# Kernel optimization log

Hardware: AMD Instinct MI355X
Metric: run time of the kernel (lower is better)

## Reference

```python
import jax, jax.numpy as jnp
import numpy as np

MD = 4  # max displacement -> (2*MD+1)**2 = 81 output channels

def setup_inputs() -> dict:
    key = jax.random.key(0)
    k1, k2 = jax.random.split(key)
    B, C, H, W = 4, 128, 128, 256
    t1 = jax.random.normal(k1, (B, C, H, W), dtype=jnp.float32)
    t2 = jax.random.normal(k2, (B, C, H, W), dtype=jnp.float32)
    return {"t1": t1, "t2": t2}

def reference(t1, t2):
    # PWC-Net correlation: for each displacement (dy,dx) in [-MD,MD]^2,
    # corr[b, d, y, x] = mean_c t1[b,c,y,x] * t2[b,c,y+dy,x+dx]
    B, C, H, W = t1.shape
    t2p = jnp.pad(t2, ((0, 0), (0, 0), (MD, MD), (MD, MD)))
    outs = []
    for dy in range(2 * MD + 1):
        for dx in range(2 * MD + 1):
            shifted = t2p[:, :, dy:dy + H, dx:dx + W]  # (B,C,H,W)
            outs.append(jnp.mean(t1 * shifted, axis=1))  # (B,H,W)
    return jnp.stack(outs, axis=1)  # (B, 81, H, W)
```

## Files before the change

kernel.cpp:

```cpp
#include <hip/hip_runtime.h>

#define MD   4
#define B_   4
#define C_   128
#define H_   128
#define W_   256
#define ND   9

typedef float  float4v __attribute__((ext_vector_type(4)));
typedef float  f32x4   __attribute__((ext_vector_type(4)));
typedef short  bf16x8  __attribute__((ext_vector_type(8)));
typedef unsigned int u32;
typedef u32    u32x4   __attribute__((ext_vector_type(4)));

#define TS ((size_t)B_ * H_ * 4 * W_ * 32)

static __device__ __forceinline__ unsigned short f2bf(float f) {
    u32 u = __float_as_uint(f);
    u32 r = (u + 0x7fffu + ((u >> 16) & 1u)) >> 16;
    return (unsigned short)r;
}

__global__ __launch_bounds__(256, 2)
void convert_one(const float* __restrict__ src0,
                 unsigned short* __restrict__ dst0) {
    const int bid = blockIdx.x;
    const int kc  = bid & 3;
    const int y   = (bid >> 2) & (H_ - 1);
    const int b   = bid >> 9;
    const int x   = threadIdx.x;
    const float* src = src0 + ((size_t)(b * C_ + kc * 32) * H_ + y) * W_ + x;
    const size_t hw = (size_t)H_ * W_;

    float f[32];
    #pragma unroll
    for (int k = 0; k < 32; ++k) f[k] = src[(size_t)k * hw];

    unsigned short* dst =
        dst0 + ((((size_t)(b * H_ + y)) * 4 + kc) * W_ + x) * 32;
    #pragma unroll
    for (int q = 0; q < 4; ++q) {
        u32x4 pk;
        #pragma unroll
        for (int j = 0; j < 4; ++j)
            pk[j] = (u32)f2bf(f[q * 8 + 2 * j]) |
                    ((u32)f2bf(f[q * 8 + 2 * j + 1]) << 16);
        *(u32x4*)(dst + q * 8) = pk;
    }
}

__global__ __launch_bounds__(512, 2)
void corr_mfma7(const float* __restrict__ t1,
                const unsigned short* __restrict__ t2w,
                float* __restrict__ out) {
    __shared__ float scr[8][2 * 16 * 33];
    __shared__ __align__(16) unsigned short aS[2][2][128][32];

    const int tid = threadIdx.x;
    const int l   = tid & 63;
    const int w   = tid >> 6;
    const int bid = blockIdx.x;
    const int xcd = bid & 7;
    const int xh  = xcd >> 2;
    const int ypq = xcd & 3;
    const int rst = bid >> 3;
    const int b   = rst >> 4;
    const int yp  = ypq * 16 + (rst & 15);
    const int y0  = yp * 2;
    const int ln  = l & 15;
    const int kg  = l >> 4;
    const int X0  = (xh * 8 + w) * 16;
    const float scale = 1.0f / (float)C_;
    const bf16x8 z8 = (bf16x8)(short)0;
    const size_t hw = (size_t)H_ * W_;

    const int q  = tid >> 7;
    const int xl = tid & 127;

    f32x4 aA0[ND], aA1[ND], aB0[ND], aB1[ND];
    #pragma unroll
    for (int r = 0; r < ND; ++r) {
        aA0[r] = (f32x4)0.0f; aA1[r] = (f32x4)0.0f;
        aB0[r] = (f32x4)0.0f; aB1[r] = (f32x4)0.0f;
    }

    int col0 = X0 - 8 + ln;
    int col1 = X0 + 8 + ln;
    const bool ob0 = col0 < 0;
    const bool ob1 = col1 > W_ - 1;
    col0 = ob0 ? 0 : col0;
    col1 = ob1 ? W_ - 1 : col1;

    float f[16];
#define ALOAD(kc_)                                                          \
    {                                                                       \
        _Pragma("unroll")                                                   \
        for (int i = 0; i < 16; ++i) {                                      \
            const int cl = (i >> 1) + 8 * q;                                \
            const int yy_ = i & 1;                                          \
            f[i] = t1[((size_t)(b * C_ + (kc_) * 32 + cl) * H_              \
                       + y0 + yy_) * W_ + xh * 128 + xl];                   \
        }                                                                   \
    }
#define AWRITE(buf_)                                                        \
    {                                                                       \
        bf16x8 w0, w1;                                                      \
        _Pragma("unroll")                                                   \
        for (int j = 0; j < 8; ++j) {                                       \
            w0[j] = (short)f2bf(f[2 * j]);                                  \
            w1[j] = (short)f2bf(f[2 * j + 1]);                              \
        }                                                                   \
        *(bf16x8*)&aS[buf_][0][xl][q * 8] = w0;                             \
        *(bf16x8*)&aS[buf_][1][xl][q * 8] = w1;                             \
    }

    ALOAD(0);
    AWRITE(0);
    __syncthreads();

    #pragma unroll
    for (int kc = 0; kc < 4; ++kc) {
        const int buf = kc & 1;
        if (kc < 3) ALOAD(kc + 1);

        const bf16x8 fA = *(const bf16x8*)&aS[buf][0][w * 16 + ln][kg * 8];
        const bf16x8 fB = *(const bf16x8*)&aS[buf][1][w * 16 + ln][kg * 8];

        #pragma unroll
        for (int r = 0; r < ND + 1; ++r) {
            const int row = y0 + r - MD;
            if (0 <= row && row < H_) {
                const unsigned short* b_base =
                    t2w + ((((size_t)(b * H_ + row)) * 4 + kc) * W_) * 32;
                bf16x8 b0 = *(const bf16x8*)(b_base + (size_t)col0 * 32 + kg * 8);
                bf16x8 b1 = *(const bf16x8*)(b_base + (size_t)col1 * 32 + kg * 8);
                b0 = ob0 ? z8 : b0;
                b1 = ob1 ? z8 : b1;
                if (r < ND) {
                    aA0[r] = __builtin_amdgcn_mfma_f32_16x16x32_bf16(fA, b0, aA0[r], 0, 0, 0);
                    aA1[r] = __builtin_amdgcn_mfma_f32_16x16x32_bf16(fA, b1, aA1[r], 0, 0, 0);
                }
                if (r >= 1) {
                    aB0[r-1] = __builtin_amdgcn_mfma_f32_16x16x32_bf16(fB, b0, aB0[r-1], 0, 0, 0);
                    aB1[r-1] = __builtin_amdgcn_mfma_f32_16x16x32_bf16(fB, b1, aB1[r-1], 0, 0, 0);
                }
            }
        }

        if (kc < 3) AWRITE(buf ^ 1);
        __syncthreads();
    }
#undef ALOAD
#undef AWRITE

    float* sw = scr[w];

    #pragma unroll
    for (int r = 0; r < ND; ++r) {
        const int row = y0 + r - MD;
        const bool liv = (0 <= row && row < H_);
        #pragma unroll
        for (int i = 0; i < 4; ++i) {
            sw[(kg * 4 + i) * 33 + ln]       = aA0[r][i];
            sw[528 + (kg * 4 + i) * 33 + ln] = aA1[r][i];
        }
        #pragma unroll
        for (int i = 0; i < 3; ++i) {
            const int dx = i * 4 + kg;
            if (dx < ND) {
                const int m  = ln;
                const int md = m + dx;
                const int idx = (md < 12) ? (m * 33 + md + 4)
                                          : (528 + m * 33 + md - 12);
                const float v = liv ? sw[idx] * scale : 0.0f;
                out[((((size_t)b * 81) + r * ND + dx) * H_ + y0) * W_ + X0 + m] = v;
            }
        }
    }
    #pragma unroll
    for (int r = 0; r < ND; ++r) {
        const int row = y0 + 1 + r - MD;
        const bool liv = (0 <= row && row < H_);
        #pragma unroll
        for (int i = 0; i < 4; ++i) {
            sw[(kg * 4 + i) * 33 + ln]       = aB0[r][i];
            sw[528 + (kg * 4 + i) * 33 + ln] = aB1[r][i];
        }
        #pragma unroll
        for (int i = 0; i < 3; ++i) {
            const int dx = i * 4 + kg;
            if (dx < ND) {
                const int m  = ln;
                const int md = m + dx;
                const int idx = (md < 12) ? (m * 33 + md + 4)
                                          : (528 + m * 33 + md - 12);
                const float v = liv ? sw[idx] * scale : 0.0f;
                out[((((size_t)b * 81) + r * ND + dx) * H_ + (y0 + 1)) * W_ + X0 + m] = v;
            }
        }
    }
}

__global__ __launch_bounds__(9 * 64, 3)
void corr_fallback(const float* __restrict__ t1,
                   const float* __restrict__ t2,
                   float* __restrict__ out) {
    const int tid  = threadIdx.x;
    const int lane = tid & 63;
    const int w    = tid >> 6;
    const int bid  = blockIdx.x;
    const int swz  = (bid & 7) * 32 + (bid >> 3);
    const int yp   = swz & 63;
    const int b    = swz >> 6;
    const int y0   = yp * 2;
    const int half = lane >> 5;
    const int lx   = lane & 31;
    const int x0   = lx * 8;
    const int yrow = y0 + half;
    const int yy   = yrow + w - MD;
    const bool live = (0 <= yy) && (yy < H_);
    const int  yc  = yy < 0 ? 0 : (yy > H_ - 1 ? H_ - 1 : yy);
    const float sc = live ? (1.0f / (float)C_) : 0.0f;
    const bool lm  = (lx == 0);
    const bool rm  = (lx == 31);
    const int offL = lm ? 0 : -4;
    const int offR = rm ? 0 :  8;

    float acc[ND][8];
    #pragma unroll
    for (int dx = 0; dx < ND; ++dx)
        #pragma unroll
        for (int j = 0; j < 8; ++j) acc[dx][j] = 0.0f;

    const float* p1 = t1 + (((size_t)(b * C_)) * H_ + yrow) * W_ + x0;
    const float* p2 = t2 + (((size_t)(b * C_)) * H_ + yc  ) * W_ + x0;
    const size_t chstr = (size_t)H_ * W_;

    #pragma unroll 2
    for (int c = 0; c < C_; ++c) {
        const float* pc1 = p1 + (size_t)c * chstr;
        const float* pc2 = p2 + (size_t)c * chstr;
        const float4v a0 = *(const float4v*)(pc1);
        const float4v a1 = *(const float4v*)(pc1 + 4);
        float4v wl = *(const float4v*)(pc2 + offL);
        const float4v v0 = *(const float4v*)(pc2);
        const float4v v1 = *(const float4v*)(pc2 + 4);
        float4v wr = *(const float4v*)(pc2 + offR);
        #pragma unroll
        for (int qq = 0; qq < 4; ++qq) {
            wl[qq] = lm ? 0.0f : wl[qq];
            wr[qq] = rm ? 0.0f : wr[qq];
        }
        float win[16];
        #pragma unroll
        for (int qq = 0; qq < 4; ++qq) {
            win[qq] = wl[qq]; win[4 + qq] = v0[qq];
            win[8 + qq] = v1[qq]; win[12 + qq] = wr[qq];
        }
        #pragma unroll
        for (int dx = 0; dx < ND; ++dx)
            #pragma unroll
            for (int j = 0; j < 8; ++j) {
                const float aj = (j < 4) ? a0[j] : a1[j - 4];
                acc[dx][j] = fmaf(aj, win[dx + j], acc[dx][j]);
            }
    }

    #pragma unroll
    for (int dx = 0; dx < ND; ++dx) {
        float4v o0, o1;
        #pragma unroll
        for (int j = 0; j < 4; ++j) {
            o0[j] = acc[dx][j] * sc;
            o1[j] = acc[dx][4 + j] * sc;
        }
        const size_t oidx =
            (((size_t)(b * ND * ND) + w * ND + dx) * H_ + yrow) * W_ + x0;
        *(float4v*)&out[oidx]     = o0;
        *(float4v*)&out[oidx + 4] = o1;
    }
}

extern "C" void kernel_launch(void* const* d_in, const int* in_sizes, int n_in,
                              void* d_out, int out_size, void* d_ws, size_t ws_size,
                              hipStream_t stream) {
    const float* t1 = (const float*)d_in[0];
    const float* t2 = (const float*)d_in[1];
    float* out      = (float*)d_out;
    const size_t need = TS * sizeof(unsigned short);
    if (ws_size >= need) {
        unsigned short* ws = (unsigned short*)d_ws;
        convert_one<<<dim3(B_ * H_ * 4), 256, 0, stream>>>(t2, ws);
        corr_mfma7 <<<dim3(B_ * H_), 512, 0, stream>>>(t1, ws, out);
    } else {
        corr_fallback<<<dim3(B_ * H_ / 2), 9 * 64, 0, stream>>>(t1, t2, out);
    }
}
```

Measured before the change: 69.03 us.

## Vectorize t1 staging loads, single-buffer padded LDS, and vectorize output stores

The t1 tile is now read with float4 loads over 8 consecutive x positions, where it used to be read with scalar per-channel loads. It is packed as bf16 channel pairs into a single padded LDS buffer, replacing the double buffer, and an extra barrier guards reuse of that buffer. The epilogue stages each displacement row in LDS so it can be written out with float4 stores instead of scalar stores. The aim is to cut global load and store instruction counts and LDS use, at the cost of one more __syncthreads per chunk and less overlap between staging and MFMA work.

```diff
diff --git a/kernel.cpp b/kernel.cpp
--- a/kernel.cpp
+++ b/kernel.cpp
@@ -50,11 +50,11 @@
 }
 
 __global__ __launch_bounds__(512, 2)
-void corr_mfma7(const float* __restrict__ t1,
+void corr_mfma8(const float* __restrict__ t1,
                 const unsigned short* __restrict__ t2w,
                 float* __restrict__ out) {
-    __shared__ float scr[8][2 * 16 * 33];
-    __shared__ __align__(16) unsigned short aS[2][2][128][32];
+    __shared__ u32   aS[2][128][20];
+    __shared__ float scr[8][16 * 36 + 9 * 16];
 
     const int tid = threadIdx.x;
     const int l   = tid & 63;
@@ -74,8 +74,31 @@
     const bf16x8 z8 = (bf16x8)(short)0;
     const size_t hw = (size_t)H_ * W_;
 
-    const int q  = tid >> 7;
-    const int xl = tid & 127;
+    const int cpair = tid & 15;
+    const int ys    = (tid >> 4) & 1;
+    const int xoct  = tid >> 5;
+    const int gx    = xh * 128 + xoct * 8;
+
+    float fst[16];
+#define ALOAD(kc_)                                                         \
+    {                                                                      \
+        const float* s0 = t1 + ((size_t)(b * C_ + (kc_) * 32 + 2 * cpair)  \
+                                * H_ + y0 + ys) * W_ + gx;                 \
+        const float* s1 = s0 + hw;                                         \
+        *(float4v*)&fst[0]  = *(const float4v*)(s0);                       \
+        *(float4v*)&fst[4]  = *(const float4v*)(s0 + 4);                   \
+        *(float4v*)&fst[8]  = *(const float4v*)(s1);                       \
+        *(float4v*)&fst[12] = *(const float4v*)(s1 + 4);                   \
+    }
+#define AWRITE()                                                           \
+    {                                                                      \
+        _Pragma("unroll")                                                  \
+        for (int j = 0; j < 8; ++j) {                                      \
+            const u32 pk = (u32)f2bf(fst[j]) |                             \
+                           ((u32)f2bf(fst[8 + j]) << 16);                  \
+            aS[ys][xoct * 8 + j][cpair] = pk;                              \
+        }                                                                  \
+    }
 
     f32x4 aA0[ND], aA1[ND], aB0[ND], aB1[ND];
     #pragma unroll
@@ -91,40 +114,14 @@
     col0 = ob0 ? 0 : col0;
     col1 = ob1 ? W_ - 1 : col1;
 
-    float f[16];
-#define ALOAD(kc_)                                                          \
-    {                                                                       \
-        _Pragma("unroll")                                                   \
-        for (int i = 0; i < 16; ++i) {                                      \
-            const int cl = (i >> 1) + 8 * q;                                \
-            const int yy_ = i & 1;                                          \
-            f[i] = t1[((size_t)(b * C_ + (kc_) * 32 + cl) * H_              \
-                       + y0 + yy_) * W_ + xh * 128 + xl];                   \
-        }                                                                   \
-    }
-#define AWRITE(buf_)                                                        \
-    {                                                                       \
-        bf16x8 w0, w1;                                                      \
-        _Pragma("unroll")                                                   \
-        for (int j = 0; j < 8; ++j) {                                       \
-            w0[j] = (short)f2bf(f[2 * j]);                                  \
-            w1[j] = (short)f2bf(f[2 * j + 1]);                              \
-        }                                                                   \
-        *(bf16x8*)&aS[buf_][0][xl][q * 8] = w0;                             \
-        *(bf16x8*)&aS[buf_][1][xl][q * 8] = w1;                             \
-    }
-
-    ALOAD(0);
-    AWRITE(0);
+    ALOAD(0); AWRITE();
     __syncthreads();
 
     #pragma unroll
     for (int kc = 0; kc < 4; ++kc) {
-        const int buf = kc & 1;
+        const bf16x8 fA = *(const bf16x8*)&aS[0][w * 16 + ln][kg * 4];
+        const bf16x8 fB = *(const bf16x8*)&aS[1][w * 16 + ln][kg * 4];
         if (kc < 3) ALOAD(kc + 1);
-
-        const bf16x8 fA = *(const bf16x8*)&aS[buf][0][w * 16 + ln][kg * 8];
-        const bf16x8 fB = *(const bf16x8*)&aS[buf][1][w * 16 + ln][kg * 8];
 
         #pragma unroll
         for (int r = 0; r < ND + 1; ++r) {
@@ -147,13 +144,15 @@
             }
         }
 
-        if (kc < 3) AWRITE(buf ^ 1);
+        __syncthreads();
+        if (kc < 3) { AWRITE(); }
         __syncthreads();
     }
 #undef ALOAD
 #undef AWRITE
 
     float* sw = scr[w];
+    float* sb = sw + 16 * 36;
 
     #pragma unroll
     for (int r = 0; r < ND; ++r) {
@@ -161,20 +160,22 @@
         const bool liv = (0 <= row && row < H_);
         #pragma unroll
         for (int i = 0; i < 4; ++i) {
-            sw[(kg * 4 + i) * 33 + ln]       = aA0[r][i];
-            sw[528 + (kg * 4 + i) * 33 + ln] = aA1[r][i];
+            sw[(kg * 4 + i) * 36 + ln]      = aA0[r][i];
+            sw[(kg * 4 + i) * 36 + 16 + ln] = aA1[r][i];
         }
         #pragma unroll
         for (int i = 0; i < 3; ++i) {
             const int dx = i * 4 + kg;
             if (dx < ND) {
-                const int m  = ln;
-                const int md = m + dx;
-                const int idx = (md < 12) ? (m * 33 + md + 4)
-                                          : (528 + m * 33 + md - 12);
-                const float v = liv ? sw[idx] * scale : 0.0f;
-                out[((((size_t)b * 81) + r * ND + dx) * H_ + y0) * W_ + X0 + m] = v;
+                const float v = liv ? sw[ln * 36 + ln + dx + 4] * scale : 0.0f;
+                sb[dx * 16 + ln] = v;
             }
+        }
+        if (l < 36) {
+            const int dxs = l >> 2, mq = l & 3;
+            const float4v v4 = *(const float4v*)&sb[dxs * 16 + mq * 4];
+            *(float4v*)&out[((((size_t)b * 81) + r * ND + dxs) * H_ + y0) * W_
+                            + X0 + mq * 4] = v4;
         }
     }
     #pragma unroll
@@ -183,20 +184,22 @@
         const bool liv = (0 <= row && row < H_);
         #pragma unroll
         for (int i = 0; i < 4; ++i) {
-            sw[(kg * 4 + i) * 33 + ln]       = aB0[r][i];
-            sw[528 + (kg * 4 + i) * 33 + ln] = aB1[r][i];
+            sw[(kg * 4 + i) * 36 + ln]      = aB0[r][i];
+            sw[(kg * 4 + i) * 36 + 16 + ln] = aB1[r][i];
         }
         #pragma unroll
         for (int i = 0; i < 3; ++i) {
             const int dx = i * 4 + kg;
             if (dx < ND) {
-                const int m  = ln;
-                const int md = m + dx;
-                const int idx = (md < 12) ? (m * 33 + md + 4)
-                                          : (528 + m * 33 + md - 12);
-                const float v = liv ? sw[idx] * scale : 0.0f;
-                out[((((size_t)b * 81) + r * ND + dx) * H_ + (y0 + 1)) * W_ + X0 + m] = v;
+                const float v = liv ? sw[ln * 36 + ln + dx + 4] * scale : 0.0f;
+                sb[dx * 16 + ln] = v;
             }
+        }
+        if (l < 36) {
+            const int dxs = l >> 2, mq = l & 3;
+            const float4v v4 = *(const float4v*)&sb[dxs * 16 + mq * 4];
+            *(float4v*)&out[((((size_t)b * 81) + r * ND + dxs) * H_ + (y0 + 1)) * W_
+                            + X0 + mq * 4] = v4;
         }
     }
 }
@@ -291,7 +294,7 @@
     if (ws_size >= need) {
         unsigned short* ws = (unsigned short*)d_ws;
         convert_one<<<dim3(B_ * H_ * 4), 256, 0, stream>>>(t2, ws);
-        corr_mfma7 <<<dim3(B_ * H_), 512, 0, stream>>>(t1, ws, out);
+        corr_mfma8 <<<dim3(B_ * H_), 512, 0, stream>>>(t1, ws, out);
     } else {
         corr_fallback<<<dim3(B_ * H_ / 2), 9 * 64, 0, stream>>>(t1, t2, out);
     }
```

Result: slower. 72.81 us (+5.5%).
